# Kernel tuning notes

Measured on AMD Instinct MI355X. Metric: run time of the kernel, lower is better.

## Reference

```python
import jax, jax.numpy as jnp
import numpy as np

DM = 768            # d_model
DI = 1536           # d_inner = expand * d_model
P = 64              # headdim
H = DI // P         # 24 heads
N = 64              # d_state (Mamba2Simple default)
K = 4               # d_conv
CONVD = DI + 2 * N  # 1664
D_IN_PROJ = 2 * DI + 2 * N + H  # 3224
BATCH = 2
NVAL = 1024
L = NVAL
EPS = 1e-5

# static tail_order / swap_order index (transpose the rows x cols token grid, reversed)
_rows = int(NVAL ** 0.5)
_t = np.arange(NVAL).reshape(_rows, -1).T
_t = NVAL - 1 - _t
TAIL = _t.reshape(-1)
SEQ = jnp.asarray(np.concatenate([np.arange(L - NVAL), TAIL + (L - NVAL)]))


def _make_params(key, prefix):
    ks = jax.random.split(key, 6)
    dt = jnp.exp(jax.random.uniform(ks[2], (H,), minval=np.log(1e-3), maxval=np.log(1e-1)))
    return {
        prefix + 'ln_w': jnp.ones(DM, jnp.float32),
        prefix + 'ln_b': jnp.zeros(DM, jnp.float32),
        prefix + 'in_w': jax.random.normal(ks[0], (D_IN_PROJ, DM), jnp.float32) * 0.02,
        prefix + 'conv_w': jax.random.normal(ks[1], (CONVD, K), jnp.float32) * 0.1,
        prefix + 'conv_b': jnp.zeros(CONVD, jnp.float32),
        prefix + 'dt_bias': jnp.log(jnp.expm1(dt)),  # inverse softplus of dt in [1e-3, 1e-1]
        prefix + 'A_log': jnp.log(jax.random.uniform(ks[3], (H,), minval=1.0, maxval=16.0)),
        prefix + 'D': jnp.ones(H, jnp.float32),
        prefix + 'norm_w': jnp.ones(DI, jnp.float32),
        prefix + 'out_w': jax.random.normal(ks[4], (DM, DI), jnp.float32) * 0.02,
    }


def setup_inputs() -> dict:
    key = jax.random.key(0)
    k1, k2, k3 = jax.random.split(key, 3)
    inp = {'x': jax.random.normal(k1, (BATCH, L, DM), dtype=jnp.float32)}
    inp.update(_make_params(k2, 'f_'))
    inp.update(_make_params(k3, 'b_'))
    return inp


def _layernorm(x, w, b):
    m = jnp.mean(x, -1, keepdims=True)
    v = jnp.mean((x - m) ** 2, -1, keepdims=True)
    return (x - m) * jax.lax.rsqrt(v + EPS) * w + b


def _mamba2(x, in_w, conv_w, conv_b, dt_bias, A_log, Dp, norm_w, out_w):
    Bsz, Lseq, _ = x.shape
    zxbcdt = x @ in_w.T                                   # [B,L,3224]
    z, xBC, dt = jnp.split(zxbcdt, [DI, DI + CONVD], axis=-1)
    dt = jax.nn.softplus(dt + dt_bias)                    # [B,L,H]
    # causal depthwise conv1d over channels
    xc = jnp.transpose(xBC, (0, 2, 1))                    # [B,C,L]
    xc = jax.lax.conv_general_dilated(xc, conv_w[:, None, :], (1,), [(K - 1, 0)],
                                      feature_group_count=CONVD)
    xBC = jax.nn.silu(jnp.transpose(xc, (0, 2, 1)) + conv_b)
    xs, Bm, Cm = jnp.split(xBC, [DI, DI + N], axis=-1)
    xs = xs.reshape(Bsz, Lseq, H, P)
    A = -jnp.exp(A_log)                                   # [H], negative

    def step(S, inp):
        dt_t, x_t, B_t, C_t = inp                         # [B,H],[B,H,P],[B,N],[B,N]
        dA = jnp.exp(dt_t * A)                            # [B,H]
        S = S * dA[..., None, None] + dt_t[..., None, None] * B_t[:, None, :, None] * x_t[:, :, None, :]
        y = jnp.einsum('bn,bhnp->bhp', C_t, S)
        return S, y

    S0 = jnp.zeros((Bsz, H, N, P), x.dtype)
    ins = (jnp.moveaxis(dt, 1, 0), jnp.moveaxis(xs, 1, 0),
           jnp.moveaxis(Bm, 1, 0), jnp.moveaxis(Cm, 1, 0))
    _, ys = jax.lax.scan(step, S0, ins)
    y = jnp.moveaxis(ys, 0, 1) + Dp[None, None, :, None] * xs  # D skip, [B,L,H,P]
    y = y.reshape(Bsz, Lseq, DI)
    # RMSNormGated: gate then rmsnorm
    y = y * jax.nn.silu(z)
    y = y * jax.lax.rsqrt(jnp.mean(y * y, -1, keepdims=True) + EPS) * norm_w
    return y @ out_w.T


def _wrap(x, ln_w, ln_b, *mp):
    return x + _mamba2(_layernorm(x, ln_w, ln_b), *mp)


def reference(x,
              f_ln_w, f_ln_b, f_in_w, f_conv_w, f_conv_b, f_dt_bias, f_A_log, f_D, f_norm_w, f_out_w,
              b_ln_w, b_ln_b, b_in_w, b_conv_w, b_conv_b, b_dt_bias, b_A_log, b_D, b_norm_w, b_out_w):
    left_right = _wrap(x, f_ln_w, f_ln_b, f_in_w, f_conv_w, f_conv_b, f_dt_bias, f_A_log, f_D, f_norm_w, f_out_w)
    xs = x[:, SEQ]
    down_up = _wrap(xs, b_ln_w, b_ln_b, b_in_w, b_conv_w, b_conv_b, b_dt_bias, b_A_log, b_D, b_norm_w, b_out_w)
    down_up = down_up[:, SEQ]
    return left_right + down_up
```

## Files before the change

kernel.cpp:

```cpp
#include <hip/hip_runtime.h>
#include <cstdint>

#define DM    768
#define DI    1536
#define PP    64
#define HH    24
#define NN    64
#define NP1   3328
#define LL    1024
#define ROWS  2048
#define DINP  3224
#define EPSF  1e-5f
#define NCHUNK 16
#define CLEN   64

typedef unsigned short ushortT;
typedef __attribute__((ext_vector_type(8))) __bf16 bf16x8;
typedef __attribute__((ext_vector_type(8))) unsigned short ushort8;
typedef __attribute__((ext_vector_type(4))) unsigned short ushort4v;
typedef __attribute__((ext_vector_type(4))) float f32x4;

__device__ __forceinline__ int seqmap(int t) { return 1023 - 32 * (t & 31) - (t >> 5); }

__device__ __forceinline__ ushortT f2bf(float f) {
  union { float f; unsigned u; } v; v.f = f;
  unsigned r = v.u + 0x7FFF + ((v.u >> 16) & 1);
  return (ushortT)(r >> 16);
}
__device__ __forceinline__ float bf2f(ushortT b) {
  union { unsigned u; float f; } v; v.u = ((unsigned)b) << 16;
  return v.f;
}

__device__ __forceinline__ void gload_lds16(const void* g, void* l) {
  __builtin_amdgcn_global_load_lds((const __attribute__((address_space(1))) void*)g,
                                   (__attribute__((address_space(3))) void*)l, 16, 0, 0);
}

#define SWZ(r, c) ((r) * 64 + ((c) ^ (((r) & 7) << 3)))
#define SWZ64(r, c) ((r) * 64 + ((c) ^ (((r) & 7) << 3)))

__global__ __launch_bounds__(256) void prep_kernel(const float* __restrict__ x,
    const float* __restrict__ wf, const float* __restrict__ bf_,
    const float* __restrict__ wb, const float* __restrict__ bb,
    ushortT* __restrict__ xln, float* __restrict__ out,
    const float* __restrict__ fw1, const float* __restrict__ bw1,
    const float* __restrict__ fw2, const float* __restrict__ bw2,
    ushortT* __restrict__ WP1, ushortT* __restrict__ W2) {
  __shared__ float lds[4];
  int bid = blockIdx.x;
  int tid = threadIdx.x;
  if (bid < 2048) {
    int b = bid >> 10, sr = bid & 1023;
    const float* xr = x + (size_t)bid * DM;
    float v0 = xr[tid], v1 = xr[tid + 256], v2 = xr[tid + 512];
    float* outp = out + (size_t)bid * DM;
    outp[tid] = 2.f * v0; outp[tid + 256] = 2.f * v1; outp[tid + 512] = 2.f * v2;
    float s = v0 + v1 + v2;
    #pragma unroll
    for (int o = 32; o; o >>= 1) s += __shfl_xor(s, o, 64);
    if ((tid & 63) == 0) lds[tid >> 6] = s;
    __syncthreads();
    float mean = (lds[0] + lds[1] + lds[2] + lds[3]) * (1.f / 768.f);
    __syncthreads();
    float d0 = v0 - mean, d1 = v1 - mean, d2 = v2 - mean;
    float q = d0 * d0 + d1 * d1 + d2 * d2;
    #pragma unroll
    for (int o = 32; o; o >>= 1) q += __shfl_xor(q, o, 64);
    if ((tid & 63) == 0) lds[tid >> 6] = q;
    __syncthreads();
    float var = (lds[0] + lds[1] + lds[2] + lds[3]) * (1.f / 768.f);
    float rs = rsqrtf(var + EPSF);
    int t1 = seqmap(sr);
    ushortT* o0 = xln + (size_t)bid * DM;
    ushortT* o1 = xln + (size_t)(2048 + b * 1024 + t1) * DM;
    o0[tid]       = f2bf(d0 * rs * wf[tid]       + bf_[tid]);
    o0[tid + 256] = f2bf(d1 * rs * wf[tid + 256] + bf_[tid + 256]);
    o0[tid + 512] = f2bf(d2 * rs * wf[tid + 512] + bf_[tid + 512]);
    o1[tid]       = f2bf(d0 * rs * wb[tid]       + bb[tid]);
    o1[tid + 256] = f2bf(d1 * rs * wb[tid + 256] + bb[tid + 256]);
    o1[tid + 512] = f2bf(d2 * rs * wb[tid + 512] + bb[tid + 512]);
  } else {
    const long NW1 = (long)NP1 * DM, SW1 = (long)DINP * DM, NW2 = (long)DM * DI;
    const long tot8 = (2 * NW1 + 2 * NW2) >> 3;
    long nb = (long)gridDim.x - 2048;
    for (long i8 = (long)(bid - 2048) * 256 + tid; i8 < tot8; i8 += nb * 256) {
      long i = i8 << 3;
      const float* src = nullptr;
      ushortT* dst;
      if (i < NW1) {
        if (i < SW1) src = fw1 + i;
        dst = WP1 + i;
      } else if (i < 2 * NW1) {
        long j = i - NW1;
        if (j < SW1) src = bw1 + j;
        dst = WP1 + i;
      } else if (i < 2 * NW1 + NW2) {
        long j = i - 2 * NW1;
        src = fw2 + j;
        dst = W2 + j;
      } else {
        long j = i - 2 * NW1 - NW2;
        src = bw2 + j;
        dst = W2 + NW2 + j;
      }
      ushort8 o = {};
      if (src) {
        float4 a = *(const float4*)src;
        float4 b2 = *(const float4*)(src + 4);
        o[0] = f2bf(a.x);  o[1] = f2bf(a.y);  o[2] = f2bf(a.z);  o[3] = f2bf(a.w);
        o[4] = f2bf(b2.x); o[5] = f2bf(b2.y); o[6] = f2bf(b2.z); o[7] = f2bf(b2.w);
      }
      *(ushort8*)dst = o;
    }
  }
}

template<int MODE>
__global__ __launch_bounds__(256) void gemm_bf16(
    const ushortT* __restrict__ Aall, const ushortT* __restrict__ Ball,
    float* __restrict__ Cfall, ushortT* __restrict__ Cball,
    int K, int lda, int ldb, int ldc, long sA, long sB, long sCf, long sCb) {
  __shared__ ushortT sA2[2][128 * 64];
  __shared__ ushortT sB2[2][128 * 64];
  int gx = gridDim.x, gy = gridDim.y;
  int nwg = gx * gy * gridDim.z;
  int lid = blockIdx.x + gx * (blockIdx.y + gy * blockIdx.z);
  int cpx = nwg >> 3;
  int swz = (lid & 7) * cpx + (lid >> 3);
  int bx = swz % gx;
  int rest = swz / gx;
  int by = rest % gy, bz = rest / gy;
  const ushortT* A = Aall + (size_t)bz * sA;
  const ushortT* B = Ball + (size_t)bz * sB;
  int tid = threadIdx.x, lane = tid & 63, w = tid >> 6;
  int wm = w >> 1, wn = w & 1;
  int m0 = by * 128, n0 = bx * 128;
  int rA8 = lane >> 3;
  int cSw = ((lane & 7) << 3) ^ (((lane >> 3) & 7) << 3);
  f32x4 acc[4][4] = {};
  const int NT = K >> 6;
  int fr = lane & 15, kq = lane >> 4;

  auto STAGE = [&](int bf, int kt) {
    int kc = kt * 64 + cSw;
    #pragma unroll
    for (int c2 = 0; c2 < 4; ++c2) {
      int q = w * 4 + c2;
      gload_lds16(A + (size_t)(m0 + q * 8 + rA8) * lda + kc, &sA2[bf][q * 512]);
    }
    #pragma unroll
    for (int c2 = 0; c2 < 4; ++c2) {
      int q = w * 4 + c2;
      gload_lds16(B + (size_t)(n0 + q * 8 + rA8) * ldb + kc, &sB2[bf][q * 512]);
    }
  };

  STAGE(0, 0);
  int cur = 0;
  for (int kt = 0; kt < NT; ++kt) {
    if (kt + 1 < NT) {
      STAGE(cur ^ 1, kt + 1);
      asm volatile("s_waitcnt vmcnt(8)" ::: "memory");
    } else {
      asm volatile("s_waitcnt vmcnt(0)" ::: "memory");
    }
    __builtin_amdgcn_s_barrier();
    __builtin_amdgcn_sched_barrier(0);
    #pragma unroll
    for (int ks = 0; ks < 2; ++ks) {
      int kb = ks * 32 + kq * 8;
      bf16x8 af[4], bfr[4];
      #pragma unroll
      for (int i = 0; i < 4; ++i)
        af[i] = *(const bf16x8*)&sA2[cur][SWZ64(wm * 64 + i * 16 + fr, kb)];
      #pragma unroll
      for (int j = 0; j < 4; ++j)
        bfr[j] = *(const bf16x8*)&sB2[cur][SWZ64(wn * 64 + j * 16 + fr, kb)];
      #pragma unroll
      for (int i = 0; i < 4; ++i)
        #pragma unroll
        for (int j = 0; j < 4; ++j)
          acc[i][j] = __builtin_amdgcn_mfma_f32_16x16x32_bf16(af[i], bfr[j], acc[i][j], 0, 0, 0);
    }
    asm volatile("s_waitcnt lgkmcnt(0)" ::: "memory");
    __builtin_amdgcn_sched_barrier(0);
    __builtin_amdgcn_s_barrier();
    cur ^= 1;
  }
  int cr = (lane >> 4) * 4, cc = lane & 15;
  if (MODE == 1 && n0 >= 3200) {
    float* Cf = Cfall + (size_t)bz * sCf;
    #pragma unroll
    for (int i = 0; i < 4; ++i)
      #pragma unroll
      for (int j = 0; j < 4; ++j) {
        float* Cp = Cf + (size_t)(m0 + wm * 64 + i * 16 + cr) * 128 + (wn * 64 + j * 16 + cc);
        #pragma unroll
        for (int r = 0; r < 4; ++r) Cp[(size_t)r * 128] = acc[i][j][r];
      }
  } else if (MODE == 2) {
    #pragma unroll
    for (int i = 0; i < 4; ++i)
      #pragma unroll
      for (int r = 0; r < 4; ++r) {
        int mrow = m0 + wm * 64 + i * 16 + cr + r;
        int brow;
        if (bz == 0) brow = mrow;
        else { int bb2 = mrow >> 10, tt2 = mrow & 1023; brow = bb2 * 1024 + seqmap(tt2); }
        float* orow = Cfall + (size_t)brow * DM;
        #pragma unroll
        for (int j = 0; j < 4; ++j)
          atomicAdd(&orow[n0 + wn * 64 + j * 16 + cc], acc[i][j][r]);
      }
  } else {
    ushortT* Cb = Cball + (size_t)bz * sCb;
    #pragma unroll
    for (int i = 0; i < 4; ++i)
      #pragma unroll
      for (int j = 0; j < 4; ++j) {
        ushortT* Cp = Cb + (size_t)(m0 + wm * 64 + i * 16 + cr) * ldc + (n0 + wn * 64 + j * 16 + cc);
        #pragma unroll
        for (int r = 0; r < 4; ++r) Cp[(size_t)r * ldc] = f2bf(acc[i][j][r]);
      }
  }
}

__global__ __launch_bounds__(256) void convbc_kernel(const ushortT* __restrict__ zxb,
    const float* __restrict__ cwf, const float* __restrict__ cbf,
    const float* __restrict__ cwb, const float* __restrict__ cbb,
    ushortT* __restrict__ bcc) {
  __shared__ ushortT sZ[67 * 128];
  int chunk = blockIdx.x, dirb = blockIdx.y;
  int dir = dirb >> 1;
  int t0 = chunk * 64;
  size_t rowb = (size_t)dirb * 1024;
  const float* cw = dir ? cwb : cwf;
  const float* cb = dir ? cbb : cbf;
  int tid = threadIdx.x;
  for (int idx = tid; idx < 67 * 16; idx += 256) {
    int r = idx >> 4, g = idx & 15;
    int t = t0 - 3 + r;
    ushort8 v = {};
    if (t >= 0) v = *(const ushort8*)&zxb[(rowb + t) * NP1 + 3072 + g * 8];
    *(ushort8*)&sZ[r * 128 + g * 8] = v;
  }
  __syncthreads();
  ushortT* outB = bcc + ((size_t)(dirb * NCHUNK + chunk) * 2) * 4096;
  ushortT* outC = outB + 4096;
  for (int idx = tid; idx < 64 * 16; idx += 256) {
    int r = idx >> 4, g = idx & 15;
    int cc8 = g * 8;
    ushort8 x0 = *(const ushort8*)&sZ[(r + 0) * 128 + cc8];
    ushort8 x1 = *(const ushort8*)&sZ[(r + 1) * 128 + cc8];
    ushort8 x2 = *(const ushort8*)&sZ[(r + 2) * 128 + cc8];
    ushort8 x3 = *(const ushort8*)&sZ[(r + 3) * 128 + cc8];
    ushort8 o;
    #pragma unroll
    for (int e = 0; e < 8; ++e) {
      int gc = 1536 + cc8 + e;
      float a = cb[gc] + bf2f(x0[e]) * cw[gc * 4 + 0] + bf2f(x1[e]) * cw[gc * 4 + 1]
              + bf2f(x2[e]) * cw[gc * 4 + 2] + bf2f(x3[e]) * cw[gc * 4 + 3];
      o[e] = f2bf(a / (1.f + __expf(-a)));
    }
    if (cc8 < 64) *(ushort8*)&outB[SWZ(r, cc8)] = o;
    else          *(ushort8*)&outC[SWZ(r, cc8 - 64)] = o;
  }
}

__global__ __launch_bounds__(256) void ssd_chunk_kernel(const ushortT* __restrict__ zxb,
    const ushortT* __restrict__ bcc,
    const float* __restrict__ dtt,
    const float* __restrict__ cwf, const float* __restrict__ cbf,
    const float* __restrict__ cwb, const float* __restrict__ cbb,
    const float* __restrict__ dtbf, const float* __restrict__ alogf,
    const float* __restrict__ dtbb, const float* __restrict__ alogb,
    ushortT* __restrict__ xcb,
    ushortT* __restrict__ yb, ushortT* __restrict__ slocb, float* __restrict__ cwg) {
  __shared__ ushortT sCb[4096];
  __shared__ ushortT sBb[4096];
  __shared__ ushortT sXT[4096];
  __shared__ ushortT sPool[8192];
  __shared__ float clog[64];
  __shared__ float dt64[64];
  __shared__ float wv64[64];
  ushortT* sBT   = sPool;
  ushortT* sMb   = sPool + 4096;
  ushortT* sRawX = sPool;

  int gh = blockIdx.x;
  int c  = blockIdx.y;
  int dir = gh / 48;
  int rem = gh % 48;
  int b = rem / 24, h = rem % 24;
  int tid = threadIdx.x, lane = tid & 63;
  int w = tid >> 6;
  int dirb = dir * 2 + b;
  size_t rowbase = (size_t)dirb * 1024;
  int t0 = c * CLEN;
  size_t trow = rowbase + (size_t)t0;
  const float* cw   = dir ? cwb : cwf;
  const float* cb   = dir ? cbb : cbf;
  const float* dtb  = dir ? dtbb : dtbf;
  const float* alog = dir ? alogb : alogf;

  {
    const ushortT* bSrc = bcc + ((size_t)(dirb * NCHUNK + c) * 2) * 4096;
    const ushortT* cSrc = bSrc + 4096;
    #pragma unroll
    for (int ph = 0; ph < 2; ++ph) {
      int base = ph * 2048 + w * 512;
      gload_lds16(bSrc + base + lane * 8, &sBb[base]);
      gload_lds16(cSrc + base + lane * 8, &sCb[base]);
    }
  }
  for (int idx = tid; idx < 67 * 8; idx += 256) {
    int r = idx >> 3, g = idx & 7;
    int t = t0 - 3 + r;
    ushort8 v = {};
    if (t >= 0) v = *(const ushort8*)&zxb[(rowbase + t) * NP1 + 1536 + h * 64 + g * 8];
    *(ushort8*)&sRawX[r * 64 + g * 8] = v;
  }
  if (tid < 64) {
    float raw = dtt[(trow + tid) * 128 + h] + dtb[h];
    float dtv = raw > 20.f ? raw : log1pf(expf(raw));
    float ld = -expf(alog[h]) * dtv;
    float v = ld;
    #pragma unroll
    for (int o = 1; o < 64; o <<= 1) {
      float u = __shfl_up(v, o, 64);
      if (tid >= o) v += u;
    }
    float tot = __shfl(v, 63, 64);
    clog[tid] = v;
    dt64[tid] = dtv;
    wv64[tid] = dtv * __expf(tot - v);
    cwg[(trow + tid) * HH + h] = __expf(v);
  }
  __syncthreads();

  {
    int p = lane;
    int ch = h * 64 + p;
    float cbv = cb[ch];
    float w0 = cw[ch * 4], w1 = cw[ch * 4 + 1], w2 = cw[ch * 4 + 2], w3 = cw[ch * 4 + 3];
    #pragma unroll
    for (int q = 0; q < 4; ++q) {
      int t4 = w * 16 + q * 4;
      float rv[7];
      #pragma unroll
      for (int rr = 0; rr < 7; ++rr) rv[rr] = bf2f(sRawX[(t4 + rr) * 64 + p]);
      ushort4v v4;
      #pragma unroll
      for (int i = 0; i < 4; ++i) {
        float a = cbv + rv[i] * w0 + rv[i + 1] * w1 + rv[i + 2] * w2 + rv[i + 3] * w3;
        v4[i] = f2bf(a / (1.f + __expf(-a)));
      }
      int cT = t4 ^ ((p & 7) << 3);
      *(ushort4v*)&sXT[p * 64 + cT] = v4;
      #pragma unroll
      for (int i = 0; i < 4; ++i)
        xcb[(trow + t4 + i) * 1536 + ch] = v4[i];
    }
  }
  __syncthreads();

  int fr = lane & 15, kq = lane >> 4;

  {
    int n = lane;
    #pragma unroll
    for (int q = 0; q < 4; ++q) {
      int s4 = w * 16 + q * 4;
      float b0 = bf2f(sBb[SWZ(s4 + 0, n)]) * wv64[s4 + 0];
      float b1 = bf2f(sBb[SWZ(s4 + 1, n)]) * wv64[s4 + 1];
      float b2 = bf2f(sBb[SWZ(s4 + 2, n)]) * wv64[s4 + 2];
      float b3 = bf2f(sBb[SWZ(s4 + 3, n)]) * wv64[s4 + 3];
      int cT = s4 ^ ((n & 7) << 3);
      ushort4v v4 = {f2bf(b0), f2bf(b1), f2bf(b2), f2bf(b3)};
      *(ushort4v*)&sBT[n * 64 + cT] = v4;
    }
  }
  f32x4 accG[4] = {};
  #pragma unroll
  for (int kt = 0; kt < 2; ++kt) {
    int kk = kt * 32 + kq * 8;
    bf16x8 af = *(const bf16x8*)&sCb[SWZ(w * 16 + fr, kk)];
    #pragma unroll
    for (int j = 0; j < 4; ++j) {
      bf16x8 bf_ = *(const bf16x8*)&sBb[SWZ(j * 16 + fr, kk)];
      accG[j] = __builtin_amdgcn_mfma_f32_16x16x32_bf16(af, bf_, accG[j], 0, 0, 0);
    }
  }
  #pragma unroll
  for (int j = 0; j < 4; ++j) {
    int s = j * 16 + fr;
    float cls = clog[s], dtv = dt64[s];
    #pragma unroll
    for (int r = 0; r < 4; ++r) {
      int t = w * 16 + kq * 4 + r;
      float dec = (s <= t) ? __expf(clog[t] - cls) * dtv : 0.f;
      sMb[SWZ(t, s)] = f2bf(accG[j][r] * dec);
    }
  }
  __syncthreads();

  f32x4 accY[4] = {}, accS[4] = {};
  #pragma unroll
  for (int kt = 0; kt < 2; ++kt) {
    int kk = kt * 32 + kq * 8;
    bf16x8 aM = *(const bf16x8*)&sMb[SWZ(w * 16 + fr, kk)];
    bf16x8 aB = *(const bf16x8*)&sBT[SWZ(w * 16 + fr, kk)];
    #pragma unroll
    for (int j = 0; j < 4; ++j) {
      bf16x8 bx = *(const bf16x8*)&sXT[SWZ(j * 16 + fr, kk)];
      accY[j] = __builtin_amdgcn_mfma_f32_16x16x32_bf16(aM, bx, accY[j], 0, 0, 0);
      accS[j] = __builtin_amdgcn_mfma_f32_16x16x32_bf16(aB, bx, accS[j], 0, 0, 0);
    }
  }
  ushortT* spb = slocb + ((size_t)gh * NCHUNK + c) * 4096;
  #pragma unroll
  for (int j = 0; j < 4; ++j) {
    #pragma unroll
    for (int r = 0; r < 4; ++r) {
      int t = w * 16 + kq * 4 + r;
      int p = j * 16 + fr;
      yb[(trow + t) * DI + h * 64 + p] = f2bf(accY[j][r]);
      spb[t * 64 + p] = f2bf(accS[j][r]);
    }
  }
}

__global__ __launch_bounds__(256) void chunk_prefix_kernel(
    const ushortT* __restrict__ slocb, const float* __restrict__ cwg,
    ushortT* __restrict__ sinitb) {
  __shared__ float ldsT[64 * 65];
  int gh = blockIdx.x;
  int dir = gh / 48;
  int rem = gh % 48;
  int b = rem / 24, h = rem % 24;
  int tid = threadIdx.x;
  size_t rowbase = ((size_t)dir * 2 + b) * 1024;
  float R[16];
  #pragma unroll
  for (int j = 0; j < 16; ++j) R[j] = 0.f;
  for (int c = 1; c < NCHUNK; ++c) {
    float W = cwg[(rowbase + (size_t)c * CLEN - 1) * HH + h];
    const ushortT* slot = slocb + ((size_t)gh * NCHUNK + (c - 1)) * 4096;
    #pragma unroll
    for (int j = 0; j < 16; ++j) {
      int idx = j * 256 + tid, n = idx >> 6, p = idx & 63;
      R[j] = __builtin_fmaf(R[j], W, bf2f(slot[idx]));
      ldsT[n * 65 + p] = R[j];
    }
    __syncthreads();
    ushortT* outp = sinitb + ((size_t)gh * (NCHUNK - 1) + (c - 1)) * 4096;
    #pragma unroll
    for (int j = 0; j < 16; ++j) {
      int idx = j * 256 + tid, p = idx >> 6, n = idx & 63;
      outp[SWZ(p, n)] = f2bf(ldsT[n * 65 + p]);
    }
    __syncthreads();
  }
}

__global__ __launch_bounds__(256) void fixup_kernel(
    const ushortT* __restrict__ bcc, const ushortT* __restrict__ sinitb,
    const float* __restrict__ cwg, ushortT* __restrict__ yib) {
  __shared__ ushortT sCb[4096];
  __shared__ ushortT sST[4096];
  int gh = blockIdx.x;
  int c = blockIdx.y + 1;
  int dir = gh / 48;
  int rem = gh % 48;
  int b = rem / 24, h = rem % 24;
  int tid = threadIdx.x, lane = tid & 63, w = tid >> 6;
  int dirb = dir * 2 + b;
  size_t rowbase = (size_t)dirb * 1024;
  size_t trow = rowbase + (size_t)c * CLEN;
  const ushortT* cbSrc = bcc + ((size_t)(dirb * NCHUNK + c) * 2 + 1) * 4096;
  const ushortT* stSrc = sinitb + ((size_t)gh * (NCHUNK - 1) + (c - 1)) * 4096;
  #pragma unroll
  for (int ph = 0; ph < 2; ++ph) {
    int base = ph * 2048 + w * 512;
    gload_lds16(cbSrc + base + lane * 8, &sCb[base]);
    gload_lds16(stSrc + base + lane * 8, &sST[base]);
  }
  __syncthreads();
  int fr = lane & 15, kq = lane >> 4;
  f32x4 accY[4] = {};
  #pragma unroll
  for (int kt = 0; kt < 2; ++kt) {
    int kk = kt * 32 + kq * 8;
    bf16x8 aC = *(const bf16x8*)&sCb[SWZ(w * 16 + fr, kk)];
    #pragma unroll
    for (int j = 0; j < 4; ++j) {
      bf16x8 bS = *(const bf16x8*)&sST[SWZ(j * 16 + fr, kk)];
      accY[j] = __builtin_amdgcn_mfma_f32_16x16x32_bf16(aC, bS, accY[j], 0, 0, 0);
    }
  }
  float cwv[4];
  #pragma unroll
  for (int r = 0; r < 4; ++r)
    cwv[r] = cwg[(trow + w * 16 + kq * 4 + r) * HH + h];
  #pragma unroll
  for (int j = 0; j < 4; ++j)
    #pragma unroll
    for (int r = 0; r < 4; ++r) {
      int t = w * 16 + kq * 4 + r, p = j * 16 + fr;
      yib[(trow + t) * DI + h * 64 + p] = f2bf(accY[j][r] * cwv[r]);
    }
}

__global__ __launch_bounds__(192) void gate_norm_kernel(
    const ushortT* __restrict__ yb, const ushortT* __restrict__ yib,
    const ushortT* __restrict__ zxb, const ushortT* __restrict__ xcb,
    const float* __restrict__ Df, const float* __restrict__ Db,
    const float* __restrict__ nwf, const float* __restrict__ nwb,
    ushortT* __restrict__ yn) {
  __shared__ float lds[3];
  int bid = blockIdx.x;
  int dir = bid >> 11;
  int t = bid & 1023;
  const float* Dp = dir ? Db : Df;
  const float* nw = dir ? nwb : nwf;
  int tid = threadIdx.x;
  int c0 = tid * 8;
  float v[8];
  float ss = 0.f;
  {
    ushort8 yv8 = *(const ushort8*)&yb[(size_t)bid * DI + c0];
    ushort8 zv8 = *(const ushort8*)&zxb[(size_t)bid * NP1 + c0];
    ushort8 xv8 = *(const ushort8*)&xcb[(size_t)bid * 1536 + c0];
    ushort8 yi8 = {};
    bool hasI = (t >= CLEN);
    if (hasI) yi8 = *(const ushort8*)&yib[(size_t)bid * DI + c0];
    float Dv = Dp[c0 >> 6];
    #pragma unroll
    for (int e = 0; e < 8; ++e) {
      float yv = bf2f(yv8[e]) + (hasI ? bf2f(yi8[e]) : 0.f) + Dv * bf2f(xv8[e]);
      float zv = bf2f(zv8[e]);
      yv *= zv / (1.f + expf(-zv));
      v[e] = yv;
      ss += yv * yv;
    }
  }
  #pragma unroll
  for (int o = 32; o; o >>= 1) ss += __shfl_xor(ss, o, 64);
  if ((tid & 63) == 0) lds[tid >> 6] = ss;
  __syncthreads();
  float ms = (lds[0] + lds[1] + lds[2]) * (1.f / 1536.f);
  float sc = rsqrtf(ms + EPSF);
  {
    ushort8 o8;
    #pragma unroll
    for (int e = 0; e < 8; ++e) o8[e] = f2bf(v[e] * sc * nw[c0 + e]);
    *(ushort8*)&yn[(size_t)bid * DI + c0] = o8;
  }
}

extern "C" void kernel_launch(void* const* d_in, const int* in_sizes, int n_in,
                              void* d_out, int out_size, void* d_ws, size_t ws_size,
                              hipStream_t stream) {
  const float* x       = (const float*)d_in[0];
  const float* f_ln_w  = (const float*)d_in[1];
  const float* f_ln_b  = (const float*)d_in[2];
  const float* f_in_w  = (const float*)d_in[3];
  const float* f_cw    = (const float*)d_in[4];
  const float* f_cb    = (const float*)d_in[5];
  const float* f_dtb   = (const float*)d_in[6];
  const float* f_alog  = (const float*)d_in[7];
  const float* f_D     = (const float*)d_in[8];
  const float* f_nw    = (const float*)d_in[9];
  const float* f_ow    = (const float*)d_in[10];
  const float* b_ln_w  = (const float*)d_in[11];
  const float* b_ln_b  = (const float*)d_in[12];
  const float* b_in_w  = (const float*)d_in[13];
  const float* b_cw    = (const float*)d_in[14];
  const float* b_cb    = (const float*)d_in[15];
  const float* b_dtb   = (const float*)d_in[16];
  const float* b_alog  = (const float*)d_in[17];
  const float* b_D     = (const float*)d_in[18];
  const float* b_nw    = (const float*)d_in[19];
  const float* b_ow    = (const float*)d_in[20];
  float* out = (float*)d_out;

  char* ws = (char*)d_ws;
  size_t off = 0;
  auto carve = [&](size_t bytes) -> char* {
    off = (off + 255) & ~(size_t)255;
    char* p = ws + off;
    off += bytes;
    return p;
  };
  ushortT* XLN   = (ushortT*)carve((size_t)2 * ROWS * DM * 2);
  ushortT* WP1   = (ushortT*)carve((size_t)2 * NP1 * DM * 2);
  ushortT* W2    = (ushortT*)carve((size_t)2 * DM * DI * 2);
  ushortT* ZXB   = (ushortT*)carve((size_t)2 * ROWS * NP1 * 2);
  float*   DTT   = (float*)carve((size_t)2 * ROWS * 128 * 4);
  ushortT* XCB   = (ushortT*)carve((size_t)2 * ROWS * 1536 * 2);
  ushortT* YB    = (ushortT*)carve((size_t)2 * ROWS * DI * 2);
  ushortT* YIB   = (ushortT*)carve((size_t)2 * ROWS * DI * 2);
  ushortT* YN    = (ushortT*)carve((size_t)2 * ROWS * DI * 2);
  ushortT* SLOCB = (ushortT*)carve((size_t)96 * NCHUNK * 4096 * 2);
  ushortT* SINIB = (ushortT*)carve((size_t)96 * (NCHUNK - 1) * 4096 * 2);
  ushortT* BCC   = (ushortT*)carve((size_t)4 * NCHUNK * 2 * 4096 * 2);
  float*   CWG   = (float*)carve((size_t)2 * ROWS * HH * 4);

  prep_kernel<<<4096, 256, 0, stream>>>(x, f_ln_w, f_ln_b, b_ln_w, b_ln_b, XLN, out,
                                        f_in_w, b_in_w, f_ow, b_ow, WP1, W2);

  gemm_bf16<1><<<dim3(NP1 / 128, ROWS / 128, 2), 256, 0, stream>>>(
      XLN, WP1, DTT, ZXB, DM, DM, DM, NP1,
      (long)ROWS * DM, (long)NP1 * DM, (long)ROWS * 128, (long)ROWS * NP1);

  convbc_kernel<<<dim3(NCHUNK, 4), 256, 0, stream>>>(ZXB, f_cw, f_cb, b_cw, b_cb, BCC);

  ssd_chunk_kernel<<<dim3(96, NCHUNK), 256, 0, stream>>>(
      ZXB, BCC, DTT, f_cw, f_cb, b_cw, b_cb, f_dtb, f_alog, b_dtb, b_alog,
      XCB, YB, SLOCB, CWG);

  chunk_prefix_kernel<<<96, 256, 0, stream>>>(SLOCB, CWG, SINIB);
  fixup_kernel<<<dim3(96, NCHUNK - 1), 256, 0, stream>>>(BCC, SINIB, CWG, YIB);

  gate_norm_kernel<<<4096, 192, 0, stream>>>(YB, YIB, ZXB, XCB, f_D, b_D, f_nw, b_nw, YN);

  gemm_bf16<2><<<dim3(DM / 128, ROWS / 128, 2), 256, 0, stream>>>(
      YN, W2, out, nullptr, DI, DI, DI, DM,
      (long)ROWS * DI, (long)DM * DI, 0, 0);
}
```

Baseline: 148.2 us.

## Fold D skip into SSD output and accumulate fixup in place, drop XCB/YIB buffers

The D·x skip term is now added in the chunk SSD kernel from the conv output already held in shared memory, so the conv output no longer has to be written to global memory. The fixup kernel adds its inter-chunk contribution directly into the y buffer (read-modify-write) instead of writing a separate buffer, and gate_norm reads one y buffer instead of three. The raw-x staging stride is padded from 64 to 72 to cut LDS bank conflicts. This saves global traffic, at the cost of rounding y to bf16 twice and a read-modify-write in fixup.

```diff
diff --git a/kernel.cpp b/kernel.cpp
--- a/kernel.cpp
+++ b/kernel.cpp
@@ -275,7 +275,7 @@
     const float* __restrict__ cwb, const float* __restrict__ cbb,
     const float* __restrict__ dtbf, const float* __restrict__ alogf,
     const float* __restrict__ dtbb, const float* __restrict__ alogb,
-    ushortT* __restrict__ xcb,
+    const float* __restrict__ Df, const float* __restrict__ Db,
     ushortT* __restrict__ yb, ushortT* __restrict__ slocb, float* __restrict__ cwg) {
   __shared__ ushortT sCb[4096];
   __shared__ ushortT sBb[4096];
@@ -303,6 +303,7 @@
   const float* cb   = dir ? cbb : cbf;
   const float* dtb  = dir ? dtbb : dtbf;
   const float* alog = dir ? alogb : alogf;
+  float Dv = (dir ? Db : Df)[h];
 
   {
     const ushortT* bSrc = bcc + ((size_t)(dirb * NCHUNK + c) * 2) * 4096;
@@ -319,7 +320,7 @@
     int t = t0 - 3 + r;
     ushort8 v = {};
     if (t >= 0) v = *(const ushort8*)&zxb[(rowbase + t) * NP1 + 1536 + h * 64 + g * 8];
-    *(ushort8*)&sRawX[r * 64 + g * 8] = v;
+    *(ushort8*)&sRawX[r * 72 + g * 8] = v;
   }
   if (tid < 64) {
     float raw = dtt[(trow + tid) * 128 + h] + dtb[h];
@@ -349,7 +350,7 @@
       int t4 = w * 16 + q * 4;
       float rv[7];
       #pragma unroll
-      for (int rr = 0; rr < 7; ++rr) rv[rr] = bf2f(sRawX[(t4 + rr) * 64 + p]);
+      for (int rr = 0; rr < 7; ++rr) rv[rr] = bf2f(sRawX[(t4 + rr) * 72 + p]);
       ushort4v v4;
       #pragma unroll
       for (int i = 0; i < 4; ++i) {
@@ -358,9 +359,6 @@
       }
       int cT = t4 ^ ((p & 7) << 3);
       *(ushort4v*)&sXT[p * 64 + cT] = v4;
-      #pragma unroll
-      for (int i = 0; i < 4; ++i)
-        xcb[(trow + t4 + i) * 1536 + ch] = v4[i];
     }
   }
   __syncthreads();
@@ -425,7 +423,8 @@
     for (int r = 0; r < 4; ++r) {
       int t = w * 16 + kq * 4 + r;
       int p = j * 16 + fr;
-      yb[(trow + t) * DI + h * 64 + p] = f2bf(accY[j][r]);
+      float xval = bf2f(sXT[SWZ(p, t)]);
+      yb[(trow + t) * DI + h * 64 + p] = f2bf(accY[j][r] + Dv * xval);
       spb[t * 64 + p] = f2bf(accS[j][r]);
     }
   }
@@ -466,7 +465,7 @@
 
 __global__ __launch_bounds__(256) void fixup_kernel(
     const ushortT* __restrict__ bcc, const ushortT* __restrict__ sinitb,
-    const float* __restrict__ cwg, ushortT* __restrict__ yib) {
+    const float* __restrict__ cwg, ushortT* __restrict__ yb) {
   __shared__ ushortT sCb[4096];
   __shared__ ushortT sST[4096];
   int gh = blockIdx.x;
@@ -508,21 +507,19 @@
     #pragma unroll
     for (int r = 0; r < 4; ++r) {
       int t = w * 16 + kq * 4 + r, p = j * 16 + fr;
-      yib[(trow + t) * DI + h * 64 + p] = f2bf(accY[j][r] * cwv[r]);
+      size_t yi = (trow + t) * DI + h * 64 + p;
+      yb[yi] = f2bf(bf2f(yb[yi]) + accY[j][r] * cwv[r]);
     }
 }
 
 __global__ __launch_bounds__(192) void gate_norm_kernel(
-    const ushortT* __restrict__ yb, const ushortT* __restrict__ yib,
-    const ushortT* __restrict__ zxb, const ushortT* __restrict__ xcb,
-    const float* __restrict__ Df, const float* __restrict__ Db,
+    const ushortT* __restrict__ yb,
+    const ushortT* __restrict__ zxb,
     const float* __restrict__ nwf, const float* __restrict__ nwb,
     ushortT* __restrict__ yn) {
   __shared__ float lds[3];
   int bid = blockIdx.x;
   int dir = bid >> 11;
-  int t = bid & 1023;
-  const float* Dp = dir ? Db : Df;
   const float* nw = dir ? nwb : nwf;
   int tid = threadIdx.x;
   int c0 = tid * 8;
@@ -531,14 +528,9 @@
   {
     ushort8 yv8 = *(const ushort8*)&yb[(size_t)bid * DI + c0];
     ushort8 zv8 = *(const ushort8*)&zxb[(size_t)bid * NP1 + c0];
-    ushort8 xv8 = *(const ushort8*)&xcb[(size_t)bid * 1536 + c0];
-    ushort8 yi8 = {};
-    bool hasI = (t >= CLEN);
-    if (hasI) yi8 = *(const ushort8*)&yib[(size_t)bid * DI + c0];
-    float Dv = Dp[c0 >> 6];
     #pragma unroll
     for (int e = 0; e < 8; ++e) {
-      float yv = bf2f(yv8[e]) + (hasI ? bf2f(yi8[e]) : 0.f) + Dv * bf2f(xv8[e]);
+      float yv = bf2f(yv8[e]);
       float zv = bf2f(zv8[e]);
       yv *= zv / (1.f + expf(-zv));
       v[e] = yv;
@@ -598,9 +590,7 @@
   ushortT* W2    = (ushortT*)carve((size_t)2 * DM * DI * 2);
   ushortT* ZXB   = (ushortT*)carve((size_t)2 * ROWS * NP1 * 2);
   float*   DTT   = (float*)carve((size_t)2 * ROWS * 128 * 4);
-  ushortT* XCB   = (ushortT*)carve((size_t)2 * ROWS * 1536 * 2);
   ushortT* YB    = (ushortT*)carve((size_t)2 * ROWS * DI * 2);
-  ushortT* YIB   = (ushortT*)carve((size_t)2 * ROWS * DI * 2);
   ushortT* YN    = (ushortT*)carve((size_t)2 * ROWS * DI * 2);
   ushortT* SLOCB = (ushortT*)carve((size_t)96 * NCHUNK * 4096 * 2);
   ushortT* SINIB = (ushortT*)carve((size_t)96 * (NCHUNK - 1) * 4096 * 2);
@@ -618,12 +608,12 @@
 
   ssd_chunk_kernel<<<dim3(96, NCHUNK), 256, 0, stream>>>(
       ZXB, BCC, DTT, f_cw, f_cb, b_cw, b_cb, f_dtb, f_alog, b_dtb, b_alog,
-      XCB, YB, SLOCB, CWG);
+      f_D, b_D, YB, SLOCB, CWG);
 
   chunk_prefix_kernel<<<96, 256, 0, stream>>>(SLOCB, CWG, SINIB);
-  fixup_kernel<<<dim3(96, NCHUNK - 1), 256, 0, stream>>>(BCC, SINIB, CWG, YIB);
-
-  gate_norm_kernel<<<4096, 192, 0, stream>>>(YB, YIB, ZXB, XCB, f_D, b_D, f_nw, b_nw, YN);
+  fixup_kernel<<<dim3(96, NCHUNK - 1), 256, 0, stream>>>(BCC, SINIB, CWG, YB);
+
+  gate_norm_kernel<<<4096, 192, 0, stream>>>(YB, ZXB, f_nw, b_nw, YN);
 
   gemm_bf16<2><<<dim3(DM / 128, ROWS / 128, 2), 256, 0, stream>>>(
       YN, W2, out, nullptr, DI, DI, DI, DM,
```

New measurement: 145.8 us. Within noise of the previous version (-1.6%).
